# Kernel optimization log

Measured on AMD Instinct MI355X. Metric: run time of the kernel, lower is better.

## Reference

```python
import jax, jax.numpy as jnp
import numpy as np

N = 10000   # num_nodes
U = 64      # num_units (rnn hidden)
IN = 2      # input_dim per node
B = 16      # batch
E = 80000   # nonzeros in sparse support (avg degree 8)
F = IN + U  # input_size after concat(inputs, state)
M = 2       # num_matrices = len(supports)+1 (single laplacian support)


def setup_inputs() -> dict:
    key = jax.random.key(0)
    ks = jax.random.split(key, 17)
    inputs = jax.random.normal(ks[0], (B, N * IN), jnp.float32)
    hx = jax.random.normal(ks[1], (B, N * U), jnp.float32)
    edge_row = jax.random.randint(ks[2], (E,), 0, N, jnp.int32)
    edge_col = jax.random.randint(ks[3], (E,), 0, N, jnp.int32)
    edge_val = jax.random.normal(ks[4], (E,), jnp.float32) * 0.1  # scaled-laplacian entries
    w1_mu = jax.random.normal(ks[5], (F * M, 2 * U), jnp.float32) * 0.05
    w1_logsig = jax.random.normal(ks[6], (F * M, 2 * U), jnp.float32) * 0.1 - 3.0
    b1_mu = jnp.ones((2 * U,), jnp.float32)  # bias_start = 1.0 for gates
    b1_logsig = jax.random.normal(ks[7], (2 * U,), jnp.float32) * 0.1 - 3.0
    w2_mu = jax.random.normal(ks[8], (F * M, U), jnp.float32) * 0.05
    w2_logsig = jax.random.normal(ks[9], (F * M, U), jnp.float32) * 0.1 - 3.0
    b2_mu = jnp.zeros((U,), jnp.float32)     # bias_start = 0.0 for candidate
    b2_logsig = jax.random.normal(ks[10], (U,), jnp.float32) * 0.1 - 3.0
    eps_w1 = jax.random.normal(ks[11], (F * M, 2 * U), jnp.float32)
    eps_b1 = jax.random.normal(ks[12], (2 * U,), jnp.float32)
    eps_w2 = jax.random.normal(ks[13], (F * M, U), jnp.float32)
    eps_b2 = jax.random.normal(ks[14], (U,), jnp.float32)
    return {"inputs": inputs, "hx": hx, "edge_val": edge_val,
            "w1_mu": w1_mu, "w1_logsig": w1_logsig, "b1_mu": b1_mu, "b1_logsig": b1_logsig,
            "w2_mu": w2_mu, "w2_logsig": w2_logsig, "b2_mu": b2_mu, "b2_logsig": b2_logsig,
            "eps_w1": eps_w1, "eps_b1": eps_b1, "eps_w2": eps_w2, "eps_b2": eps_b2,
            "edge_row": edge_row, "edge_col": edge_col}


def _spmm(edge_row, edge_col, edge_val, x):
    # sparse [N,N] @ dense [N,K] via gather + segment_sum (matches torch.sparse.mm)
    msg = edge_val[:, None] * x[edge_col]          # [E, K]
    return jax.ops.segment_sum(msg, edge_row, num_segments=N)


def _gconv(inp3, st3, edge_row, edge_col, edge_val, W, b):
    # inp3 [B,N,IN], st3 [B,N,U] -> out [B,N,out]
    x0 = jnp.concatenate([inp3, st3], axis=-1)      # [B,N,F]
    f = x0.shape[-1]
    x0 = x0.transpose(1, 2, 0).reshape(N, f * B)    # [N, F*B]
    x1 = _spmm(edge_row, edge_col, edge_val, x0)    # [N, F*B]
    x = jnp.stack([x0, x1], axis=0)                 # [M,N,F*B]
    x = x.reshape(M, N, f, B).transpose(3, 1, 2, 0).reshape(B * N, f * M)
    return (x @ W + b).reshape(B, N, -1)


def reference(inputs, hx, edge_val, w1_mu, w1_logsig, b1_mu, b1_logsig,
              w2_mu, w2_logsig, b2_mu, b2_logsig,
              eps_w1, eps_b1, eps_w2, eps_b2, edge_row, edge_col):
    # BNN reparameterized weights: w = mu + exp(log_sigma) * eps
    W1 = w1_mu + jnp.exp(w1_logsig) * eps_w1
    B1 = b1_mu + jnp.exp(b1_logsig) * eps_b1
    W2 = w2_mu + jnp.exp(w2_logsig) * eps_w2
    B2 = b2_mu + jnp.exp(b2_logsig) * eps_b2

    inp3 = inputs.reshape(B, N, IN)
    hx3 = hx.reshape(B, N, U)

    # gates (reset r, update u)
    value = jax.nn.sigmoid(_gconv(inp3, hx3, edge_row, edge_col, edge_val, W1, B1))  # [B,N,2U]
    r, u = jnp.split(value, 2, axis=-1)
    r = r.reshape(B, N * U)
    u = u.reshape(B, N * U)

    # candidate state
    c = _gconv(inp3, (r * hx).reshape(B, N, U), edge_row, edge_col, edge_val, W2, B2)
    c = jnp.tanh(c.reshape(B, N * U))

    new_state = u * hx + (1.0 - u) * c
    return new_state
```

## Files before the change

### kernel.cpp

```cpp
#include <hip/hip_runtime.h>
#include <cmath>

#define N_NODES 10000
#define UNITS   64
#define IND     2
#define BATCH   16
#define NEDGE   80000
#define FDIM    66
#define OG      128
#define OC      64
#define HXS     (N_NODES*UNITS)
#define INS     (N_NODES*IND)
#define KTILES  5
#define FQ      17
#define CHUNKS  272
#define LDSC    21
#define CAP     64

typedef __attribute__((ext_vector_type(8))) short bf16x8;
typedef __attribute__((ext_vector_type(4))) float f32x4;
typedef __attribute__((ext_vector_type(2))) float f32x2;
typedef unsigned long long u64;

__device__ __forceinline__ float bf2f(unsigned short u) {
  union { unsigned u; float f; } v; v.u = ((unsigned)u) << 16; return v.f;
}
__device__ __forceinline__ unsigned short f2bf(float x) {
  union { float f; unsigned u; } v; v.f = x;
  unsigned r = v.u + 0x7fffu + ((v.u >> 16) & 1u);
  return (unsigned short)(r >> 16);
}
__device__ __forceinline__ unsigned cvt2bf(float a, float b) {
  unsigned r; asm("v_cvt_pk_bf16_f32 %0, %1, %2" : "=v"(r) : "v"(a), "v"(b)); return r;
}
__device__ __forceinline__ unsigned pk4fp8(float a, float b, float c, float d) {
  int v = __builtin_amdgcn_cvt_pk_fp8_f32(a, b, 0, false);
  v = __builtin_amdgcn_cvt_pk_fp8_f32(c, d, v, true);
  return (unsigned)v;
}
__device__ __forceinline__ unsigned char f2fp8(float a) {
  return (unsigned char)(__builtin_amdgcn_cvt_pk_fp8_f32(a, 0.f, 0, false) & 0xff);
}

__global__ __launch_bounds__(256) void prep_kernel(
    const float* __restrict__ inputs, const float* __restrict__ hx,
    const float* __restrict__ w1mu, const float* __restrict__ w1ls, const float* __restrict__ ew1,
    const float* __restrict__ b1mu, const float* __restrict__ b1ls, const float* __restrict__ eb1,
    const float* __restrict__ w2mu, const float* __restrict__ w2ls, const float* __restrict__ ew2,
    const float* __restrict__ b2mu, const float* __restrict__ b2ls, const float* __restrict__ eb2,
    const int* __restrict__ erow, const int* __restrict__ ecol, const float* __restrict__ eval,
    short* __restrict__ W1p, short* __restrict__ W2p,
    float* __restrict__ B1, float* __restrict__ B2,
    int* __restrict__ cnt, u64* __restrict__ epk,
    unsigned* __restrict__ X8, uint2* __restrict__ X0bf) {
  int blk = blockIdx.x, t = threadIdx.x;
  if (blk < 16) {
    int i = blk * 256 + t;
    if (i < 2560) {
      int l = i & 63, kt = (i >> 6) % KTILES, nt = i / (KTILES * 64);
      int o = nt * 16 + (l & 15), s = l >> 4;
      bf16x8 fr;
#pragma unroll
      for (int j = 0; j < 8; ++j) {
        int f = kt * 16 + s * 4 + (j & 3);
        int src = j >> 2;
        float w = 0.f;
        if (f < FDIM) { int idx = (2 * f + src) * OG + o; w = w1mu[idx] + __expf(w1ls[idx]) * ew1[idx]; }
        fr[j] = (short)f2bf(w);
      }
      *((bf16x8*)W1p + i) = fr;
    } else if (i < 3840) {
      int i2 = i - 2560;
      int l = i2 & 63, kt = (i2 >> 6) % KTILES, nt = i2 / (KTILES * 64);
      int o = nt * 16 + (l & 15), s = l >> 4;
      bf16x8 fr;
#pragma unroll
      for (int j = 0; j < 8; ++j) {
        int f = kt * 16 + s * 4 + (j & 3);
        int src = j >> 2;
        float w = 0.f;
        if (f < FDIM) { int idx = (2 * f + src) * OC + o; w = w2mu[idx] + __expf(w2ls[idx]) * ew2[idx]; }
        fr[j] = (short)f2bf(w);
      }
      *((bf16x8*)W2p + i2) = fr;
    } else if (i < 3968) {
      int j = i - 3840; B1[j] = b1mu[j] + __expf(b1ls[j]) * eb1[j];
    } else if (i < 4032) {
      int j = i - 3968; B2[j] = b2mu[j] + __expf(b2ls[j]) * eb2[j];
    }
  } else if (blk < 16 + 313) {
    int i = (blk - 16) * 256 + t;
    if (i < NEDGE) {
      int r = erow[i];
      int pos = atomicAdd(&cnt[r], 1);
      if (pos < CAP)
        epk[(size_t)r * CAP + pos] =
            (u64)(unsigned)(ecol[i] * CHUNKS) | ((u64)__float_as_uint(eval[i]) << 32);
    }
  } else {
    int i = (blk - 329) * 256 + t;
    if (i >= N_NODES * CHUNKS) return;
    int n = i / CHUNKS;
    int c = i - n * CHUNKS;
    int b = c / FQ;
    int fq = c - b * FQ;
    const float* hp = hx + (size_t)b * HXS + n * UNITS;
    float v0, v1, v2, v3;
    if (fq == 0) {
      const float* ip = inputs + (size_t)b * INS + n * IND;
      v0 = ip[0]; v1 = ip[1]; v2 = hp[0]; v3 = hp[1];
    } else if (fq < 16) {
      f32x2 a = *reinterpret_cast<const f32x2*>(hp + fq * 4 - 2);
      f32x2 d = *reinterpret_cast<const f32x2*>(hp + fq * 4);
      v0 = a[0]; v1 = a[1]; v2 = d[0]; v3 = d[1];
    } else {
      f32x2 a = *reinterpret_cast<const f32x2*>(hp + 62);
      v0 = a[0]; v1 = a[1]; v2 = 0.f; v3 = 0.f;
    }
    X8[i] = pk4fp8(v0, v1, v2, v3);
    X0bf[i] = make_uint2(cvt2bf(v0, v1), cvt2bf(v2, v3));
  }
}

__device__ __forceinline__ void gather_write(const unsigned* __restrict__ X8t,
                                             int deg, const u64* __restrict__ ebk,
                                             int t, unsigned ow0, unsigned ow1,
                                             unsigned ow0e, unsigned ow1e,
                                             unsigned short* Y) {
  const bool extra = t < 16;
  const int c = t, c2 = 256 + t;
  if (t < 48) {
    int b = t / 3, fqp = 17 + (t - (t / 3) * 3);
    *reinterpret_cast<uint4*>(Y + (b * LDSC + fqp) * 8) = make_uint4(0u, 0u, 0u, 0u);
  }
  f32x2 g01 = {0.f, 0.f}, g23 = {0.f, 0.f}, ge01 = {0.f, 0.f}, ge23 = {0.f, 0.f};
  const unsigned* bc = X8t + c;
  const unsigned* bc2 = X8t + c2;

  {
    unsigned o[8]; float v[8];
#pragma unroll
    for (int j = 0; j < 8; ++j) {
      u64 p = ebk[j];
      bool on = j < deg;
      o[j] = on ? (unsigned)p : 0u;
      v[j] = on ? __uint_as_float((unsigned)(p >> 32)) : 0.f;
    }
    unsigned wv[8];
#pragma unroll
    for (int j = 0; j < 8; ++j) wv[j] = bc[o[j]];
    unsigned yv[8];
    if (extra) {
#pragma unroll
      for (int j = 0; j < 8; ++j) yv[j] = bc2[o[j]];
    }
#pragma unroll
    for (int j = 0; j < 8; ++j) {
      f32x2 vv = {v[j], v[j]};
      g01 += vv * __builtin_amdgcn_cvt_pk_f32_fp8((int)wv[j], false);
      g23 += vv * __builtin_amdgcn_cvt_pk_f32_fp8((int)wv[j], true);
      if (extra) {
        ge01 += vv * __builtin_amdgcn_cvt_pk_f32_fp8((int)yv[j], false);
        ge23 += vv * __builtin_amdgcn_cvt_pk_f32_fp8((int)yv[j], true);
      }
    }
  }
  for (int e = 8; e < deg; e += 4) {
    unsigned o[4]; float v[4];
#pragma unroll
    for (int j = 0; j < 4; ++j) {
      int ee = e + j;
      u64 p = ebk[ee < CAP ? ee : CAP - 1];
      bool on = ee < deg;
      o[j] = on ? (unsigned)p : 0u;
      v[j] = on ? __uint_as_float((unsigned)(p >> 32)) : 0.f;
    }
    unsigned wv[4];
#pragma unroll
    for (int j = 0; j < 4; ++j) wv[j] = bc[o[j]];
    unsigned yv[4];
    if (extra) {
#pragma unroll
      for (int j = 0; j < 4; ++j) yv[j] = bc2[o[j]];
    }
#pragma unroll
    for (int j = 0; j < 4; ++j) {
      f32x2 vv = {v[j], v[j]};
      g01 += vv * __builtin_amdgcn_cvt_pk_f32_fp8((int)wv[j], false);
      g23 += vv * __builtin_amdgcn_cvt_pk_f32_fp8((int)wv[j], true);
      if (extra) {
        ge01 += vv * __builtin_amdgcn_cvt_pk_f32_fp8((int)yv[j], false);
        ge23 += vv * __builtin_amdgcn_cvt_pk_f32_fp8((int)yv[j], true);
      }
    }
  }

  int b = c / FQ, fq = c - (c / FQ) * FQ;
  *reinterpret_cast<uint4*>(Y + (b * LDSC + fq) * 8) =
      make_uint4(ow0, ow1, cvt2bf(g01[0], g01[1]), cvt2bf(g23[0], g23[1]));
  if (extra) {
    *reinterpret_cast<uint4*>(Y + (15 * LDSC + (t + 1)) * 8) =
        make_uint4(ow0e, ow1e, cvt2bf(ge01[0], ge01[1]), cvt2bf(ge23[0], ge23[1]));
  }
}

__device__ __forceinline__ void build_afrag(const unsigned short* Y, int ml, int s, bf16x8* af) {
#pragma unroll
  for (int kt = 0; kt < KTILES; ++kt)
    af[kt] = *reinterpret_cast<const bf16x8*>(Y + (ml * LDSC + kt * 4 + s) * 8);
}

__global__ __launch_bounds__(256) void gates_kernel(
    const uint2* __restrict__ X0bf, const unsigned* __restrict__ X8,
    const short* __restrict__ W1p, const float* __restrict__ B1,
    const int* __restrict__ cnt, const u64* __restrict__ epk,
    unsigned* __restrict__ X8c, unsigned* __restrict__ upk) {
  __shared__ __align__(16) unsigned short Y[16 * LDSC * 8];
  __shared__ __align__(16) unsigned X8s[CHUNKS];
  int n = blockIdx.x, t = threadIdx.x;
  int lane = t & 63, w = t >> 6;

  const uint2* xrow = X0bf + (size_t)n * CHUNKS;
  uint2 own = xrow[t];
  unsigned ow0 = own.x, ow1 = own.y;
  int b0 = t / FQ, fq0 = t - b0 * FQ;
  X8s[t] = (fq0 == 0)
      ? pk4fp8(bf2f((unsigned short)(ow0 & 0xffffu)), bf2f((unsigned short)(ow0 >> 16)), 0.f, 0.f)
      : 0u;
  unsigned ow0e = 0, ow1e = 0;
  if (t < 16) {
    uint2 own2 = xrow[256 + t];
    ow0e = own2.x; ow1e = own2.y;
    X8s[256 + t] = 0u;
  }

  int deg = cnt[n]; if (deg > CAP) deg = CAP;
  gather_write(X8, deg, epk + (size_t)n * CAP, t, ow0, ow1, ow0e, ow1e, Y);
  __syncthreads();

  int ml = lane & 15, s = lane >> 4;
  bf16x8 af[KTILES];
  build_afrag(Y, ml, s, af);

  const bf16x8* Wp = (const bf16x8*)W1p;
#pragma unroll
  for (int q = 0; q < 2; ++q) {
    int nt = w * 2 + q;
    f32x4 acc = {0.f, 0.f, 0.f, 0.f};
#pragma unroll
    for (int kt = 0; kt < KTILES; ++kt)
      acc = __builtin_amdgcn_mfma_f32_16x16x32_bf16(af[kt], Wp[(nt * KTILES + kt) * 64 + lane],
                                                    acc, 0, 0, 0);
    int o = nt * 16 + ml;
    float bias = B1[o];
    int f = (o < UNITS ? o : o - UNITS) + IND, fqi = f >> 2, fr = f & 3;
    if (o < UNITS) {
#pragma unroll
      for (int r = 0; r < 4; ++r) {
        int b = s * 4 + r;
        float h = bf2f(Y[(b * LDSC + fqi) * 8 + fr]);
        float sg = 1.f / (1.f + __expf(-(acc[r] + bias)));
        ((unsigned char*)X8s)[(b * FQ + fqi) * 4 + fr] = f2fp8(sg * h);
      }
    } else {
      int ou = o - UNITS;
#pragma unroll
      for (int r = 0; r < 4; ++r) {
        int b = s * 4 + r;
        float h = bf2f(Y[(b * LDSC + fqi) * 8 + fr]);
        float u = 1.f / (1.f + __expf(-(acc[r] + bias)));
        upk[(size_t)b * HXS + n * UNITS + ou] = cvt2bf(u, u * h);
      }
    }
  }
  __syncthreads();
  X8c[(size_t)n * CHUNKS + t] = X8s[t];
  if (t < 16) X8c[(size_t)n * CHUNKS + 256 + t] = X8s[256 + t];
}

__global__ __launch_bounds__(256) void cand_kernel(
    const unsigned* __restrict__ X8c, const short* __restrict__ W2p,
    const float* __restrict__ B2,
    const int* __restrict__ cnt, const u64* __restrict__ epk,
    const unsigned* __restrict__ upk, float* __restrict__ out) {
  __shared__ __align__(16) unsigned short Y[16 * LDSC * 8];
  int n = blockIdx.x, t = threadIdx.x;
  int lane = t & 63, w = t >> 6;

  const unsigned* xrow = X8c + (size_t)n * CHUNKS;
  unsigned wo = xrow[t];
  f32x2 lo = __builtin_amdgcn_cvt_pk_f32_fp8((int)wo, false);
  f32x2 hi = __builtin_amdgcn_cvt_pk_f32_fp8((int)wo, true);
  unsigned ow0 = cvt2bf(lo[0], lo[1]), ow1 = cvt2bf(hi[0], hi[1]);
  unsigned ow0e = 0, ow1e = 0;
  if (t < 16) {
    unsigned wo2 = xrow[256 + t];
    f32x2 lo2 = __builtin_amdgcn_cvt_pk_f32_fp8((int)wo2, false);
    f32x2 hi2 = __builtin_amdgcn_cvt_pk_f32_fp8((int)wo2, true);
    ow0e = cvt2bf(lo2[0], lo2[1]); ow1e = cvt2bf(hi2[0], hi2[1]);
  }

  int deg = cnt[n]; if (deg > CAP) deg = CAP;
  gather_write(X8c, deg, epk + (size_t)n * CAP, t, ow0, ow1, ow0e, ow1e, Y);
  __syncthreads();

  int ml = lane & 15, s = lane >> 4;
  bf16x8 af[KTILES];
  build_afrag(Y, ml, s, af);

  const bf16x8* Wp = (const bf16x8*)W2p;
  f32x4 acc = {0.f, 0.f, 0.f, 0.f};
#pragma unroll
  for (int kt = 0; kt < KTILES; ++kt)
    acc = __builtin_amdgcn_mfma_f32_16x16x32_bf16(af[kt], Wp[(w * KTILES + kt) * 64 + lane],
                                                  acc, 0, 0, 0);
  int o = w * 16 + ml;
  float bias = B2[o];
#pragma unroll
  for (int r = 0; r < 4; ++r) {
    int b = s * 4 + r;
    size_t idx = (size_t)b * HXS + n * UNITS + o;
    float x = acc[r] + bias;
    float c = 1.f - 2.f / (__expf(2.f * x) + 1.f);
    unsigned pk = upk[idx];
    float u = bf2f((unsigned short)(pk & 0xffffu));
    float uh = bf2f((unsigned short)(pk >> 16));
    out[idx] = uh + (1.f - u) * c;
  }
}

extern "C" void kernel_launch(void* const* d_in, const int* in_sizes, int n_in,
                              void* d_out, int out_size, void* d_ws, size_t ws_size,
                              hipStream_t stream) {
  const float* inputs = (const float*)d_in[0];
  const float* hx     = (const float*)d_in[1];
  const float* eval   = (const float*)d_in[2];
  const float* w1mu   = (const float*)d_in[3];
  const float* w1ls   = (const float*)d_in[4];
  const float* b1mu   = (const float*)d_in[5];
  const float* b1ls   = (const float*)d_in[6];
  const float* w2mu   = (const float*)d_in[7];
  const float* w2ls   = (const float*)d_in[8];
  const float* b2mu   = (const float*)d_in[9];
  const float* b2ls   = (const float*)d_in[10];
  const float* ew1    = (const float*)d_in[11];
  const float* eb1    = (const float*)d_in[12];
  const float* ew2    = (const float*)d_in[13];
  const float* eb2    = (const float*)d_in[14];
  const int* erow     = (const int*)d_in[15];
  const int* ecol     = (const int*)d_in[16];
  float* out = (float*)d_out;

  char* p = (char*)d_ws;
  short* W1p = (short*)p;                   p += 20480 * 2;
  short* W2p = (short*)p;                   p += 10240 * 2;
  float* B1  = (float*)p;                   p += 128 * 4;
  float* B2  = (float*)p;                   p += 64 * 4;
  unsigned* X8  = (unsigned*)p;             p += (size_t)N_NODES * CHUNKS * 4;
  unsigned* X8c = (unsigned*)p;             p += (size_t)N_NODES * CHUNKS * 4;
  uint2* X0bf = (uint2*)p;                  p += (size_t)N_NODES * CHUNKS * 8;
  unsigned* upk = (unsigned*)p;             p += (size_t)BATCH * HXS * 4;
  int* cnt    = (int*)p;                    p += N_NODES * 4;
  u64* epk    = (u64*)p;                    p += (size_t)N_NODES * CAP * 8;

  hipMemsetAsync(cnt, 0, N_NODES * sizeof(int), stream);
  prep_kernel<<<16 + 313 + (N_NODES * CHUNKS) / 256, 256, 0, stream>>>(
      inputs, hx, w1mu, w1ls, ew1, b1mu, b1ls, eb1,
      w2mu, w2ls, ew2, b2mu, b2ls, eb2, erow, ecol, eval,
      W1p, W2p, B1, B2, cnt, epk, X8, X0bf);
  gates_kernel<<<N_NODES, 256, 0, stream>>>(X0bf, X8, W1p, B1, cnt, epk, X8c, upk);
  cand_kernel<<<N_NODES, 256, 0, stream>>>(X8c, W2p, B2, cnt, epk, upk, out);
}
```

Baseline: 90.86 us.

## Split sparse gather into standalone SpMM kernel with chunk-sliced node grouping

Moves the neighbor gather/accumulate out of the gates and candidate kernels into a separate spmm_kernel. Each block handles 7 nodes times a 34-chunk slice, so consecutive blocks share column slices, which may improve cache locality of the fp8 gathers. The per-node GEMM kernels then read the precomputed X1 from global memory. This adds two kernel launches and an extra write and read of the bf16 X1 buffer, and leaves 18 of 256 threads idle per block.

Result: slower. 112.4 us (+23.7%).

```diff
diff --git a/kernel.cpp b/kernel.cpp
--- a/kernel.cpp
+++ b/kernel.cpp
@@ -16,6 +16,8 @@
 #define CHUNKS  272
 #define LDSC    21
 #define CAP     64
+#define SCH     34
+#define NPB     7
 
 typedef __attribute__((ext_vector_type(8))) short bf16x8;
 typedef __attribute__((ext_vector_type(4))) float f32x4;
@@ -122,21 +124,19 @@
   }
 }
 
-__device__ __forceinline__ void gather_write(const unsigned* __restrict__ X8t,
-                                             int deg, const u64* __restrict__ ebk,
-                                             int t, unsigned ow0, unsigned ow1,
-                                             unsigned ow0e, unsigned ow1e,
-                                             unsigned short* Y) {
-  const bool extra = t < 16;
-  const int c = t, c2 = 256 + t;
-  if (t < 48) {
-    int b = t / 3, fqp = 17 + (t - (t / 3) * 3);
-    *reinterpret_cast<uint4*>(Y + (b * LDSC + fqp) * 8) = make_uint4(0u, 0u, 0u, 0u);
-  }
-  f32x2 g01 = {0.f, 0.f}, g23 = {0.f, 0.f}, ge01 = {0.f, 0.f}, ge23 = {0.f, 0.f};
+__global__ __launch_bounds__(256) void spmm_kernel(
+    const unsigned* __restrict__ X8t, const int* __restrict__ cnt,
+    const u64* __restrict__ epk, uint2* __restrict__ X1) {
+  int bid = blockIdx.x, t = threadIdx.x;
+  int s = bid & 7, g = bid >> 3;
+  int nl = t / SCH, ch = t - nl * SCH;
+  int n = g * NPB + nl;
+  if (nl >= NPB || n >= N_NODES) return;
+  int c = s * SCH + ch;
+  int deg = cnt[n]; if (deg > CAP) deg = CAP;
+  const u64* ebk = epk + (size_t)n * CAP;
   const unsigned* bc = X8t + c;
-  const unsigned* bc2 = X8t + c2;
-
+  f32x2 g01 = {0.f, 0.f}, g23 = {0.f, 0.f};
   {
     unsigned o[8]; float v[8];
 #pragma unroll
@@ -149,20 +149,11 @@
     unsigned wv[8];
 #pragma unroll
     for (int j = 0; j < 8; ++j) wv[j] = bc[o[j]];
-    unsigned yv[8];
-    if (extra) {
-#pragma unroll
-      for (int j = 0; j < 8; ++j) yv[j] = bc2[o[j]];
-    }
 #pragma unroll
     for (int j = 0; j < 8; ++j) {
       f32x2 vv = {v[j], v[j]};
       g01 += vv * __builtin_amdgcn_cvt_pk_f32_fp8((int)wv[j], false);
       g23 += vv * __builtin_amdgcn_cvt_pk_f32_fp8((int)wv[j], true);
-      if (extra) {
-        ge01 += vv * __builtin_amdgcn_cvt_pk_f32_fp8((int)yv[j], false);
-        ge23 += vv * __builtin_amdgcn_cvt_pk_f32_fp8((int)yv[j], true);
-      }
     }
   }
   for (int e = 8; e < deg; e += 4) {
@@ -178,30 +169,14 @@
     unsigned wv[4];
 #pragma unroll
     for (int j = 0; j < 4; ++j) wv[j] = bc[o[j]];
-    unsigned yv[4];
-    if (extra) {
-#pragma unroll
-      for (int j = 0; j < 4; ++j) yv[j] = bc2[o[j]];
-    }
 #pragma unroll
     for (int j = 0; j < 4; ++j) {
       f32x2 vv = {v[j], v[j]};
       g01 += vv * __builtin_amdgcn_cvt_pk_f32_fp8((int)wv[j], false);
       g23 += vv * __builtin_amdgcn_cvt_pk_f32_fp8((int)wv[j], true);
-      if (extra) {
-        ge01 += vv * __builtin_amdgcn_cvt_pk_f32_fp8((int)yv[j], false);
-        ge23 += vv * __builtin_amdgcn_cvt_pk_f32_fp8((int)yv[j], true);
-      }
-    }
-  }
-
-  int b = c / FQ, fq = c - (c / FQ) * FQ;
-  *reinterpret_cast<uint4*>(Y + (b * LDSC + fq) * 8) =
-      make_uint4(ow0, ow1, cvt2bf(g01[0], g01[1]), cvt2bf(g23[0], g23[1]));
-  if (extra) {
-    *reinterpret_cast<uint4*>(Y + (15 * LDSC + (t + 1)) * 8) =
-        make_uint4(ow0e, ow1e, cvt2bf(ge01[0], ge01[1]), cvt2bf(ge23[0], ge23[1]));
-  }
+    }
+  }
+  X1[(size_t)n * CHUNKS + c] = make_uint2(cvt2bf(g01[0], g01[1]), cvt2bf(g23[0], g23[1]));
 }
 
 __device__ __forceinline__ void build_afrag(const unsigned short* Y, int ml, int s, bf16x8* af) {
@@ -211,9 +186,8 @@
 }
 
 __global__ __launch_bounds__(256) void gates_kernel(
-    const uint2* __restrict__ X0bf, const unsigned* __restrict__ X8,
+    const uint2* __restrict__ X0bf, const uint2* __restrict__ X1,
     const short* __restrict__ W1p, const float* __restrict__ B1,
-    const int* __restrict__ cnt, const u64* __restrict__ epk,
     unsigned* __restrict__ X8c, unsigned* __restrict__ upk) {
   __shared__ __align__(16) unsigned short Y[16 * LDSC * 8];
   __shared__ __align__(16) unsigned X8s[CHUNKS];
@@ -221,21 +195,26 @@
   int lane = t & 63, w = t >> 6;
 
   const uint2* xrow = X0bf + (size_t)n * CHUNKS;
+  const uint2* x1row = X1 + (size_t)n * CHUNKS;
   uint2 own = xrow[t];
-  unsigned ow0 = own.x, ow1 = own.y;
+  uint2 g1 = x1row[t];
   int b0 = t / FQ, fq0 = t - b0 * FQ;
   X8s[t] = (fq0 == 0)
-      ? pk4fp8(bf2f((unsigned short)(ow0 & 0xffffu)), bf2f((unsigned short)(ow0 >> 16)), 0.f, 0.f)
+      ? pk4fp8(bf2f((unsigned short)(own.x & 0xffffu)), bf2f((unsigned short)(own.x >> 16)), 0.f, 0.f)
       : 0u;
-  unsigned ow0e = 0, ow1e = 0;
+  if (t < 48) {
+    int b = t / 3, fqp = 17 + (t - (t / 3) * 3);
+    *reinterpret_cast<uint4*>(Y + (b * LDSC + fqp) * 8) = make_uint4(0u, 0u, 0u, 0u);
+  }
+  *reinterpret_cast<uint4*>(Y + ((t / FQ) * LDSC + fq0) * 8) =
+      make_uint4(own.x, own.y, g1.x, g1.y);
   if (t < 16) {
     uint2 own2 = xrow[256 + t];
-    ow0e = own2.x; ow1e = own2.y;
+    uint2 g1e = x1row[256 + t];
+    *reinterpret_cast<uint4*>(Y + (15 * LDSC + (t + 1)) * 8) =
+        make_uint4(own2.x, own2.y, g1e.x, g1e.y);
     X8s[256 + t] = 0u;
   }
-
-  int deg = cnt[n]; if (deg > CAP) deg = CAP;
-  gather_write(X8, deg, epk + (size_t)n * CAP, t, ow0, ow1, ow0e, ow1e, Y);
   __syncthreads();
 
   int ml = lane & 15, s = lane >> 4;
@@ -279,29 +258,34 @@
 }
 
 __global__ __launch_bounds__(256) void cand_kernel(
-    const unsigned* __restrict__ X8c, const short* __restrict__ W2p,
-    const float* __restrict__ B2,
-    const int* __restrict__ cnt, const u64* __restrict__ epk,
+    const unsigned* __restrict__ X8c, const uint2* __restrict__ X1,
+    const short* __restrict__ W2p, const float* __restrict__ B2,
     const unsigned* __restrict__ upk, float* __restrict__ out) {
   __shared__ __align__(16) unsigned short Y[16 * LDSC * 8];
   int n = blockIdx.x, t = threadIdx.x;
   int lane = t & 63, w = t >> 6;
 
   const unsigned* xrow = X8c + (size_t)n * CHUNKS;
+  const uint2* x1row = X1 + (size_t)n * CHUNKS;
   unsigned wo = xrow[t];
+  uint2 g1 = x1row[t];
   f32x2 lo = __builtin_amdgcn_cvt_pk_f32_fp8((int)wo, false);
   f32x2 hi = __builtin_amdgcn_cvt_pk_f32_fp8((int)wo, true);
-  unsigned ow0 = cvt2bf(lo[0], lo[1]), ow1 = cvt2bf(hi[0], hi[1]);
-  unsigned ow0e = 0, ow1e = 0;
+  if (t < 48) {
+    int b = t / 3, fqp = 17 + (t - (t / 3) * 3);
+    *reinterpret_cast<uint4*>(Y + (b * LDSC + fqp) * 8) = make_uint4(0u, 0u, 0u, 0u);
+  }
+  int b0 = t / FQ, fq0 = t - b0 * FQ;
+  *reinterpret_cast<uint4*>(Y + (b0 * LDSC + fq0) * 8) =
+      make_uint4(cvt2bf(lo[0], lo[1]), cvt2bf(hi[0], hi[1]), g1.x, g1.y);
   if (t < 16) {
     unsigned wo2 = xrow[256 + t];
+    uint2 g1e = x1row[256 + t];
     f32x2 lo2 = __builtin_amdgcn_cvt_pk_f32_fp8((int)wo2, false);
     f32x2 hi2 = __builtin_amdgcn_cvt_pk_f32_fp8((int)wo2, true);
-    ow0e = cvt2bf(lo2[0], lo2[1]); ow1e = cvt2bf(hi2[0], hi2[1]);
-  }
-
-  int deg = cnt[n]; if (deg > CAP) deg = CAP;
-  gather_write(X8c, deg, epk + (size_t)n * CAP, t, ow0, ow1, ow0e, ow1e, Y);
+    *reinterpret_cast<uint4*>(Y + (15 * LDSC + (t + 1)) * 8) =
+        make_uint4(cvt2bf(lo2[0], lo2[1]), cvt2bf(hi2[0], hi2[1]), g1e.x, g1e.y);
+  }
   __syncthreads();
 
   int ml = lane & 15, s = lane >> 4;
@@ -359,15 +343,19 @@
   unsigned* X8  = (unsigned*)p;             p += (size_t)N_NODES * CHUNKS * 4;
   unsigned* X8c = (unsigned*)p;             p += (size_t)N_NODES * CHUNKS * 4;
   uint2* X0bf = (uint2*)p;                  p += (size_t)N_NODES * CHUNKS * 8;
+  uint2* X1   = (uint2*)p;                  p += (size_t)N_NODES * CHUNKS * 8;
   unsigned* upk = (unsigned*)p;             p += (size_t)BATCH * HXS * 4;
   int* cnt    = (int*)p;                    p += N_NODES * 4;
   u64* epk    = (u64*)p;                    p += (size_t)N_NODES * CAP * 8;
 
+  int spmm_grid = 8 * ((N_NODES + NPB - 1) / NPB);
   hipMemsetAsync(cnt, 0, N_NODES * sizeof(int), stream);
   prep_kernel<<<16 + 313 + (N_NODES * CHUNKS) / 256, 256, 0, stream>>>(
       inputs, hx, w1mu, w1ls, ew1, b1mu, b1ls, eb1,
       w2mu, w2ls, ew2, b2mu, b2ls, eb2, erow, ecol, eval,
       W1p, W2p, B1, B2, cnt, epk, X8, X0bf);
-  gates_kernel<<<N_NODES, 256, 0, stream>>>(X0bf, X8, W1p, B1, cnt, epk, X8c, upk);
-  cand_kernel<<<N_NODES, 256, 0, stream>>>(X8c, W2p, B2, cnt, epk, upk, out);
-}
+  spmm_kernel<<<spmm_grid, 256, 0, stream>>>(X8, cnt, epk, X1);
+  gates_kernel<<<N_NODES, 256, 0, stream>>>(X0bf, X1, W1p, B1, X8c, upk);
+  spmm_kernel<<<spmm_grid, 256, 0, stream>>>(X8c, cnt, epk, X1);
+  cand_kernel<<<N_NODES, 256, 0, stream>>>(X8c, X1, W2p, B2, upk, out);
+}
```

## Process two nodes per block in gates and candidate kernels

Applied to the files above, without the earlier changes.

Each block of the gates and candidate kernels now handles two adjacent nodes instead of one, and the grid is halved. The first eight edge gathers for both nodes are issued together to raise memory-level parallelism, and the weight fragments for the MFMA stage are reused across the two nodes. The cost is more registers and twice the shared memory per block, which may lower occupancy, and each block now waits on the slower of its two nodes' degree tails.

After: 93.33 us. +2.7%, slower.

```diff
diff --git a/kernel.cpp b/kernel.cpp
--- a/kernel.cpp
+++ b/kernel.cpp
@@ -122,56 +122,85 @@
   }
 }
 
-__device__ __forceinline__ void gather_write(const unsigned* __restrict__ X8t,
-                                             int deg, const u64* __restrict__ ebk,
-                                             int t, unsigned ow0, unsigned ow1,
-                                             unsigned ow0e, unsigned ow1e,
-                                             unsigned short* Y) {
+__device__ __forceinline__ void gather2(const unsigned* __restrict__ X8t,
+                                        int degA, const u64* __restrict__ ebkA,
+                                        int degB, const u64* __restrict__ ebkB,
+                                        int t,
+                                        unsigned owA0, unsigned owA1,
+                                        unsigned owA0e, unsigned owA1e,
+                                        unsigned owB0, unsigned owB1,
+                                        unsigned owB0e, unsigned owB1e,
+                                        unsigned short* YA, unsigned short* YB) {
   const bool extra = t < 16;
   const int c = t, c2 = 256 + t;
   if (t < 48) {
     int b = t / 3, fqp = 17 + (t - (t / 3) * 3);
-    *reinterpret_cast<uint4*>(Y + (b * LDSC + fqp) * 8) = make_uint4(0u, 0u, 0u, 0u);
-  }
-  f32x2 g01 = {0.f, 0.f}, g23 = {0.f, 0.f}, ge01 = {0.f, 0.f}, ge23 = {0.f, 0.f};
+    *reinterpret_cast<uint4*>(YA + (b * LDSC + fqp) * 8) = make_uint4(0u, 0u, 0u, 0u);
+    *reinterpret_cast<uint4*>(YB + (b * LDSC + fqp) * 8) = make_uint4(0u, 0u, 0u, 0u);
+  }
   const unsigned* bc = X8t + c;
   const unsigned* bc2 = X8t + c2;
 
-  {
-    unsigned o[8]; float v[8];
-#pragma unroll
-    for (int j = 0; j < 8; ++j) {
-      u64 p = ebk[j];
-      bool on = j < deg;
-      o[j] = on ? (unsigned)p : 0u;
-      v[j] = on ? __uint_as_float((unsigned)(p >> 32)) : 0.f;
-    }
-    unsigned wv[8];
-#pragma unroll
-    for (int j = 0; j < 8; ++j) wv[j] = bc[o[j]];
-    unsigned yv[8];
+  u64 pA[8], pB[8];
+#pragma unroll
+  for (int j = 0; j < 8; ++j) pA[j] = ebkA[j];
+#pragma unroll
+  for (int j = 0; j < 8; ++j) pB[j] = ebkB[j];
+  unsigned oA[8], oB[8]; float vA[8], vB[8];
+#pragma unroll
+  for (int j = 0; j < 8; ++j) {
+    bool on = j < degA;
+    oA[j] = on ? (unsigned)pA[j] : 0u;
+    vA[j] = on ? __uint_as_float((unsigned)(pA[j] >> 32)) : 0.f;
+  }
+#pragma unroll
+  for (int j = 0; j < 8; ++j) {
+    bool on = j < degB;
+    oB[j] = on ? (unsigned)pB[j] : 0u;
+    vB[j] = on ? __uint_as_float((unsigned)(pB[j] >> 32)) : 0.f;
+  }
+  unsigned wA[8], wB[8];
+#pragma unroll
+  for (int j = 0; j < 8; ++j) wA[j] = bc[oA[j]];
+#pragma unroll
+  for (int j = 0; j < 8; ++j) wB[j] = bc[oB[j]];
+  unsigned yA[8], yB[8];
+  if (extra) {
+#pragma unroll
+    for (int j = 0; j < 8; ++j) yA[j] = bc2[oA[j]];
+#pragma unroll
+    for (int j = 0; j < 8; ++j) yB[j] = bc2[oB[j]];
+  }
+
+  f32x2 gA01 = {0.f, 0.f}, gA23 = {0.f, 0.f}, geA01 = {0.f, 0.f}, geA23 = {0.f, 0.f};
+  f32x2 gB01 = {0.f, 0.f}, gB23 = {0.f, 0.f}, geB01 = {0.f, 0.f}, geB23 = {0.f, 0.f};
+#pragma unroll
+  for (int j = 0; j < 8; ++j) {
+    f32x2 vv = {vA[j], vA[j]};
+    gA01 += vv * __builtin_amdgcn_cvt_pk_f32_fp8((int)wA[j], false);
+    gA23 += vv * __builtin_amdgcn_cvt_pk_f32_fp8((int)wA[j], true);
     if (extra) {
-#pragma unroll
-      for (int j = 0; j < 8; ++j) yv[j] = bc2[o[j]];
-    }
-#pragma unroll
-    for (int j = 0; j < 8; ++j) {
-      f32x2 vv = {v[j], v[j]};
-      g01 += vv * __builtin_amdgcn_cvt_pk_f32_fp8((int)wv[j], false);
-      g23 += vv * __builtin_amdgcn_cvt_pk_f32_fp8((int)wv[j], true);
-      if (extra) {
-        ge01 += vv * __builtin_amdgcn_cvt_pk_f32_fp8((int)yv[j], false);
-        ge23 += vv * __builtin_amdgcn_cvt_pk_f32_fp8((int)yv[j], true);
-      }
-    }
-  }
-  for (int e = 8; e < deg; e += 4) {
+      geA01 += vv * __builtin_amdgcn_cvt_pk_f32_fp8((int)yA[j], false);
+      geA23 += vv * __builtin_amdgcn_cvt_pk_f32_fp8((int)yA[j], true);
+    }
+  }
+#pragma unroll
+  for (int j = 0; j < 8; ++j) {
+    f32x2 vv = {vB[j], vB[j]};
+    gB01 += vv * __builtin_amdgcn_cvt_pk_f32_fp8((int)wB[j], false);
+    gB23 += vv * __builtin_amdgcn_cvt_pk_f32_fp8((int)wB[j], true);
+    if (extra) {
+      geB01 += vv * __builtin_amdgcn_cvt_pk_f32_fp8((int)yB[j], false);
+      geB23 += vv * __builtin_amdgcn_cvt_pk_f32_fp8((int)yB[j], true);
+    }
+  }
+  for (int e = 8; e < degA; e += 4) {
     unsigned o[4]; float v[4];
 #pragma unroll
     for (int j = 0; j < 4; ++j) {
       int ee = e + j;
-      u64 p = ebk[ee < CAP ? ee : CAP - 1];
-      bool on = ee < deg;
+      u64 p = ebkA[ee < CAP ? ee : CAP - 1];
+      bool on = ee < degA;
       o[j] = on ? (unsigned)p : 0u;
       v[j] = on ? __uint_as_float((unsigned)(p >> 32)) : 0.f;
     }
@@ -186,21 +215,54 @@
 #pragma unroll
     for (int j = 0; j < 4; ++j) {
       f32x2 vv = {v[j], v[j]};
-      g01 += vv * __builtin_amdgcn_cvt_pk_f32_fp8((int)wv[j], false);
-      g23 += vv * __builtin_amdgcn_cvt_pk_f32_fp8((int)wv[j], true);
+      gA01 += vv * __builtin_amdgcn_cvt_pk_f32_fp8((int)wv[j], false);
+      gA23 += vv * __builtin_amdgcn_cvt_pk_f32_fp8((int)wv[j], true);
       if (extra) {
-        ge01 += vv * __builtin_amdgcn_cvt_pk_f32_fp8((int)yv[j], false);
-        ge23 += vv * __builtin_amdgcn_cvt_pk_f32_fp8((int)yv[j], true);
+        geA01 += vv * __builtin_amdgcn_cvt_pk_f32_fp8((int)yv[j], false);
+        geA23 += vv * __builtin_amdgcn_cvt_pk_f32_fp8((int)yv[j], true);
       }
     }
   }
+  for (int e = 8; e < degB; e += 4) {
+    unsigned o[4]; float v[4];
+#pragma unroll
+    for (int j = 0; j < 4; ++j) {
+      int ee = e + j;
+      u64 p = ebkB[ee < CAP ? ee : CAP - 1];
+      bool on = ee < degB;
+      o[j] = on ? (unsigned)p : 0u;
+      v[j] = on ? __uint_as_float((unsigned)(p >> 32)) : 0.f;
+    }
+    unsigned wv[4];
+#pragma unroll
+    for (int j = 0; j < 4; ++j) wv[j] = bc[o[j]];
+    unsigned yv[4];
+    if (extra) {
+#pragma unroll
+      for (int j = 0; j < 4; ++j) yv[j] = bc2[o[j]];
+    }
+#pragma unroll
+    for (int j = 0; j < 4; ++j) {
+      f32x2 vv = {v[j], v[j]};
+      gB01 += vv * __builtin_amdgcn_cvt_pk_f32_fp8((int)wv[j], false);
+      gB23 += vv * __builtin_amdgcn_cvt_pk_f32_fp8((int)wv[j], true);
+      if (extra) {
+        geB01 += vv * __builtin_amdgcn_cvt_pk_f32_fp8((int)yv[j], false);
+        geB23 += vv * __builtin_amdgcn_cvt_pk_f32_fp8((int)yv[j], true);
+      }
+    }
+  }
 
   int b = c / FQ, fq = c - (c / FQ) * FQ;
-  *reinterpret_cast<uint4*>(Y + (b * LDSC + fq) * 8) =
-      make_uint4(ow0, ow1, cvt2bf(g01[0], g01[1]), cvt2bf(g23[0], g23[1]));
+  *reinterpret_cast<uint4*>(YA + (b * LDSC + fq) * 8) =
+      make_uint4(owA0, owA1, cvt2bf(gA01[0], gA01[1]), cvt2bf(gA23[0], gA23[1]));
+  *reinterpret_cast<uint4*>(YB + (b * LDSC + fq) * 8) =
+      make_uint4(owB0, owB1, cvt2bf(gB01[0], gB01[1]), cvt2bf(gB23[0], gB23[1]));
   if (extra) {
-    *reinterpret_cast<uint4*>(Y + (15 * LDSC + (t + 1)) * 8) =
-        make_uint4(ow0e, ow1e, cvt2bf(ge01[0], ge01[1]), cvt2bf(ge23[0], ge23[1]));
+    *reinterpret_cast<uint4*>(YA + (15 * LDSC + (t + 1)) * 8) =
+        make_uint4(owA0e, owA1e, cvt2bf(geA01[0], geA01[1]), cvt2bf(geA23[0], geA23[1]));
+    *reinterpret_cast<uint4*>(YB + (15 * LDSC + (t + 1)) * 8) =
+        make_uint4(owB0e, owB1e, cvt2bf(geB01[0], geB01[1]), cvt2bf(geB23[0], geB23[1]));
   }
 }
 
@@ -215,67 +277,81 @@
     const short* __restrict__ W1p, const float* __restrict__ B1,
     const int* __restrict__ cnt, const u64* __restrict__ epk,
     unsigned* __restrict__ X8c, unsigned* __restrict__ upk) {
-  __shared__ __align__(16) unsigned short Y[16 * LDSC * 8];
-  __shared__ __align__(16) unsigned X8s[CHUNKS];
-  int n = blockIdx.x, t = threadIdx.x;
+  __shared__ __align__(16) unsigned short Y[2][16 * LDSC * 8];
+  __shared__ __align__(16) unsigned X8s[2][CHUNKS];
+  int t = threadIdx.x;
   int lane = t & 63, w = t >> 6;
-
-  const uint2* xrow = X0bf + (size_t)n * CHUNKS;
-  uint2 own = xrow[t];
-  unsigned ow0 = own.x, ow1 = own.y;
+  int nA = 2 * blockIdx.x, nB = nA + 1;
+
+  const uint2* xrA = X0bf + (size_t)nA * CHUNKS;
+  const uint2* xrB = X0bf + (size_t)nB * CHUNKS;
+  uint2 ownA = xrA[t], ownB = xrB[t];
   int b0 = t / FQ, fq0 = t - b0 * FQ;
-  X8s[t] = (fq0 == 0)
-      ? pk4fp8(bf2f((unsigned short)(ow0 & 0xffffu)), bf2f((unsigned short)(ow0 >> 16)), 0.f, 0.f)
+  X8s[0][t] = (fq0 == 0)
+      ? pk4fp8(bf2f((unsigned short)(ownA.x & 0xffffu)), bf2f((unsigned short)(ownA.x >> 16)), 0.f, 0.f)
       : 0u;
-  unsigned ow0e = 0, ow1e = 0;
+  X8s[1][t] = (fq0 == 0)
+      ? pk4fp8(bf2f((unsigned short)(ownB.x & 0xffffu)), bf2f((unsigned short)(ownB.x >> 16)), 0.f, 0.f)
+      : 0u;
+  unsigned owA0e = 0, owA1e = 0, owB0e = 0, owB1e = 0;
   if (t < 16) {
-    uint2 own2 = xrow[256 + t];
-    ow0e = own2.x; ow1e = own2.y;
-    X8s[256 + t] = 0u;
-  }
-
-  int deg = cnt[n]; if (deg > CAP) deg = CAP;
-  gather_write(X8, deg, epk + (size_t)n * CAP, t, ow0, ow1, ow0e, ow1e, Y);
+    uint2 a2 = xrA[256 + t], b2 = xrB[256 + t];
+    owA0e = a2.x; owA1e = a2.y; owB0e = b2.x; owB1e = b2.y;
+    X8s[0][256 + t] = 0u; X8s[1][256 + t] = 0u;
+  }
+
+  int degA = cnt[nA]; if (degA > CAP) degA = CAP;
+  int degB = cnt[nB]; if (degB > CAP) degB = CAP;
+  gather2(X8, degA, epk + (size_t)nA * CAP, degB, epk + (size_t)nB * CAP, t,
+          ownA.x, ownA.y, owA0e, owA1e, ownB.x, ownB.y, owB0e, owB1e, Y[0], Y[1]);
   __syncthreads();
 
   int ml = lane & 15, s = lane >> 4;
-  bf16x8 af[KTILES];
-  build_afrag(Y, ml, s, af);
-
   const bf16x8* Wp = (const bf16x8*)W1p;
 #pragma unroll
-  for (int q = 0; q < 2; ++q) {
-    int nt = w * 2 + q;
-    f32x4 acc = {0.f, 0.f, 0.f, 0.f};
-#pragma unroll
-    for (int kt = 0; kt < KTILES; ++kt)
-      acc = __builtin_amdgcn_mfma_f32_16x16x32_bf16(af[kt], Wp[(nt * KTILES + kt) * 64 + lane],
-                                                    acc, 0, 0, 0);
-    int o = nt * 16 + ml;
-    float bias = B1[o];
-    int f = (o < UNITS ? o : o - UNITS) + IND, fqi = f >> 2, fr = f & 3;
-    if (o < UNITS) {
-#pragma unroll
-      for (int r = 0; r < 4; ++r) {
-        int b = s * 4 + r;
-        float h = bf2f(Y[(b * LDSC + fqi) * 8 + fr]);
-        float sg = 1.f / (1.f + __expf(-(acc[r] + bias)));
-        ((unsigned char*)X8s)[(b * FQ + fqi) * 4 + fr] = f2fp8(sg * h);
+  for (int nn = 0; nn < 2; ++nn) {
+    int n = nA + nn;
+    const unsigned short* Yn = Y[nn];
+    bf16x8 af[KTILES];
+    build_afrag(Yn, ml, s, af);
+#pragma unroll
+    for (int q = 0; q < 2; ++q) {
+      int nt = w * 2 + q;
+      f32x4 acc = {0.f, 0.f, 0.f, 0.f};
+#pragma unroll
+      for (int kt = 0; kt < KTILES; ++kt)
+        acc = __builtin_amdgcn_mfma_f32_16x16x32_bf16(af[kt], Wp[(nt * KTILES + kt) * 64 + lane],
+                                                      acc, 0, 0, 0);
+      int o = nt * 16 + ml;
+      float bias = B1[o];
+      int f = (o < UNITS ? o : o - UNITS) + IND, fqi = f >> 2, fr = f & 3;
+      if (o < UNITS) {
+#pragma unroll
+        for (int r = 0; r < 4; ++r) {
+          int b = s * 4 + r;
+          float h = bf2f(Yn[(b * LDSC + fqi) * 8 + fr]);
+          float sg = 1.f / (1.f + __expf(-(acc[r] + bias)));
+          ((unsigned char*)X8s[nn])[(b * FQ + fqi) * 4 + fr] = f2fp8(sg * h);
+        }
+      } else {
+        int ou = o - UNITS;
+#pragma unroll
+        for (int r = 0; r < 4; ++r) {
+          int b = s * 4 + r;
+          float h = bf2f(Yn[(b * LDSC + fqi) * 8 + fr]);
+          float u = 1.f / (1.f + __expf(-(acc[r] + bias)));
+          upk[(size_t)b * HXS + n * UNITS + ou] = cvt2bf(u, u * h);
+        }
       }
-    } else {
-      int ou = o - UNITS;
-#pragma unroll
-      for (int r = 0; r < 4; ++r) {
-        int b = s * 4 + r;
-        float h = bf2f(Y[(b * LDSC + fqi) * 8 + fr]);
-        float u = 1.f / (1.f + __expf(-(acc[r] + bias)));
-        upk[(size_t)b * HXS + n * UNITS + ou] = cvt2bf(u, u * h);
-      }
     }
   }
   __syncthreads();
-  X8c[(size_t)n * CHUNKS + t] = X8s[t];
-  if (t < 16) X8c[(size_t)n * CHUNKS + 256 + t] = X8s[256 + t];
+#pragma unroll
+  for (int nn = 0; nn < 2; ++nn) {
+    int n = nA + nn;
+    X8c[(size_t)n * CHUNKS + t] = X8s[nn][t];
+    if (t < 16) X8c[(size_t)n * CHUNKS + 256 + t] = X8s[nn][256 + t];
+  }
 }
 
 __global__ __launch_bounds__(256) void cand_kernel(
@@ -283,49 +359,62 @@
     const float* __restrict__ B2,
     const int* __restrict__ cnt, const u64* __restrict__ epk,
     const unsigned* __restrict__ upk, float* __restrict__ out) {
-  __shared__ __align__(16) unsigned short Y[16 * LDSC * 8];
-  int n = blockIdx.x, t = threadIdx.x;
+  __shared__ __align__(16) unsigned short Y[2][16 * LDSC * 8];
+  int t = threadIdx.x;
   int lane = t & 63, w = t >> 6;
-
-  const unsigned* xrow = X8c + (size_t)n * CHUNKS;
-  unsigned wo = xrow[t];
-  f32x2 lo = __builtin_amdgcn_cvt_pk_f32_fp8((int)wo, false);
-  f32x2 hi = __builtin_amdgcn_cvt_pk_f32_fp8((int)wo, true);
-  unsigned ow0 = cvt2bf(lo[0], lo[1]), ow1 = cvt2bf(hi[0], hi[1]);
-  unsigned ow0e = 0, ow1e = 0;
+  int nA = 2 * blockIdx.x, nB = nA + 1;
+
+  const unsigned* xrA = X8c + (size_t)nA * CHUNKS;
+  const unsigned* xrB = X8c + (size_t)nB * CHUNKS;
+  unsigned woA = xrA[t], woB = xrB[t];
+  f32x2 loA = __builtin_amdgcn_cvt_pk_f32_fp8((int)woA, false);
+  f32x2 hiA = __builtin_amdgcn_cvt_pk_f32_fp8((int)woA, true);
+  f32x2 loB = __builtin_amdgcn_cvt_pk_f32_fp8((int)woB, false);
+  f32x2 hiB = __builtin_amdgcn_cvt_pk_f32_fp8((int)woB, true);
+  unsigned owA0 = cvt2bf(loA[0], loA[1]), owA1 = cvt2bf(hiA[0], hiA[1]);
+  unsigned owB0 = cvt2bf(loB[0], loB[1]), owB1 = cvt2bf(hiB[0], hiB[1]);
+  unsigned owA0e = 0, owA1e = 0, owB0e = 0, owB1e = 0;
   if (t < 16) {
-    unsigned wo2 = xrow[256 + t];
-    f32x2 lo2 = __builtin_amdgcn_cvt_pk_f32_fp8((int)wo2, false);
-    f32x2 hi2 = __builtin_amdgcn_cvt_pk_f32_fp8((int)wo2, true);
-    ow0e = cvt2bf(lo2[0], lo2[1]); ow1e = cvt2bf(hi2[0], hi2[1]);
-  }
-
-  int deg = cnt[n]; if (deg > CAP) deg = CAP;
-  gather_write(X8c, deg, epk + (size_t)n * CAP, t, ow0, ow1, ow0e, ow1e, Y);
+    unsigned wa2 = xrA[256 + t], wb2 = xrB[256 + t];
+    f32x2 la = __builtin_amdgcn_cvt_pk_f32_fp8((int)wa2, false);
+    f32x2 ha = __builtin_amdgcn_cvt_pk_f32_fp8((int)wa2, true);
+    f32x2 lb = __builtin_amdgcn_cvt_pk_f32_fp8((int)wb2, false);
+    f32x2 hb = __builtin_amdgcn_cvt_pk_f32_fp8((int)wb2, true);
+    owA0e = cvt2bf(la[0], la[1]); owA1e = cvt2bf(ha[0], ha[1]);
+    owB0e = cvt2bf(lb[0], lb[1]); owB1e = cvt2bf(hb[0], hb[1]);
+  }
+
+  int degA = cnt[nA]; if (degA > CAP) degA = CAP;
+  int degB = cnt[nB]; if (degB > CAP) degB = CAP;
+  gather2(X8c, degA, epk + (size_t)nA * CAP, degB, epk + (size_t)nB * CAP, t,
+          owA0, owA1, owA0e, owA1e, owB0, owB1, owB0e, owB1e, Y[0], Y[1]);
   __syncthreads();
 
   int ml = lane & 15, s = lane >> 4;
-  bf16x8 af[KTILES];
-  build_afrag(Y, ml, s, af);
-
   const bf16x8* Wp = (const bf16x8*)W2p;
-  f32x4 acc = {0.f, 0.f, 0.f, 0.f};
-#pragma unroll
-  for (int kt = 0; kt < KTILES; ++kt)
-    acc = __builtin_amdgcn_mfma_f32_16x16x32_bf16(af[kt], Wp[(w * KTILES + kt) * 64 + lane],
-                                                  acc, 0, 0, 0);
-  int o = w * 16 + ml;
-  float bias = B2[o];
-#pragma unroll
-  for (int r = 0; r < 4; ++r) {
-    int b = s * 4 + r;
-    size_t idx = (size_t)b * HXS + n * UNITS + o;
-    float x = acc[r] + bias;
-    float c = 1.f - 2.f / (__expf(2.f * x) + 1.f);
-    unsigned pk = upk[idx];
-    float u = bf2f((unsigned short)(pk & 0xffffu));
-    float uh = bf2f((unsigned short)(pk >> 16));
-    out[idx] = uh + (1.f - u) * c;
+#pragma unroll
+  for (int nn = 0; nn < 2; ++nn) {
+    int n = nA + nn;
+    bf16x8 af[KTILES];
+    build_afrag(Y[nn], ml, s, af);
+    f32x4 acc = {0.f, 0.f, 0.f, 0.f};
+#pragma unroll
+    for (int kt = 0; kt < KTILES; ++kt)
+      acc = __builtin_amdgcn_mfma_f32_16x16x32_bf16(af[kt], Wp[(w * KTILES + kt) * 64 + lane],
+                                                    acc, 0, 0, 0);
+    int o = w * 16 + ml;
+    float bias = B2[o];
+#pragma unroll
+    for (int r = 0; r < 4; ++r) {
+      int b = s * 4 + r;
+      size_t idx = (size_t)b * HXS + n * UNITS + o;
+      float x = acc[r] + bias;
+      float c = 1.f - 2.f / (__expf(2.f * x) + 1.f);
+      unsigned pk = upk[idx];
+      float u = bf2f((unsigned short)(pk & 0xffffu));
+      float uh = bf2f((unsigned short)(pk >> 16));
+      out[idx] = uh + (1.f - u) * c;
+    }
   }
 }
 
@@ -368,6 +457,6 @@
       inputs, hx, w1mu, w1ls, ew1, b1mu, b1ls, eb1,
       w2mu, w2ls, ew2, b2mu, b2ls, eb2, erow, ecol, eval,
       W1p, W2p, B1, B2, cnt, epk, X8, X0bf);
-  gates_kernel<<<N_NODES, 256, 0, stream>>>(X0bf, X8, W1p, B1, cnt, epk, X8c, upk);
-  cand_kernel<<<N_NODES, 256, 0, stream>>>(X8c, W2p, B2, cnt, epk, upk, out);
-}
+  gates_kernel<<<N_NODES / 2, 256, 0, stream>>>(X0bf, X8, W1p, B1, cnt, epk, X8c, upk);
+  cand_kernel<<<N_NODES / 2, 256, 0, stream>>>(X8c, W2p, B2, cnt, epk, upk, out);
+}
```
